# Optimization experiments

Measured on AMD Instinct MI355X. Metric: run time of the kernel, lower is better.

The kernel has to match this reference:

```python
import jax, jax.numpy as jnp
from jax import lax
import numpy as np

B, S, D = 4, 4096, 1024
ESCAPE_RADIUS = 2.0  # Mandelbrot-style escape bound used for per-row clamping
EPS = 1e-12


def setup_inputs() -> dict:
    key = jax.random.key(0)
    ks = jax.random.split(key, 6)
    x = jax.random.normal(ks[0], (B, S, D), dtype=jnp.float32)
    gamma = jnp.ones((D,), dtype=jnp.float32)
    beta = jnp.zeros((D,), dtype=jnp.float32)
    scale = 1.0 / np.sqrt(D)
    W_in = jax.random.normal(ks[1], (D, D), dtype=jnp.float32) * scale
    b_in = jnp.zeros((D,), dtype=jnp.float32)
    W_out = jax.random.normal(ks[2], (D, D), dtype=jnp.float32) * scale
    b_out = jnp.zeros((D,), dtype=jnp.float32)
    return {"x": x, "gamma": gamma, "beta": beta, "W_in": W_in,
            "b_in": b_in, "W_out": W_out, "b_out": b_out}


def _layernorm(x, gamma, beta):
    mu = jnp.mean(x, axis=-1, keepdims=True)
    var = jnp.mean((x - mu) ** 2, axis=-1, keepdims=True)
    return (x - mu) * lax.rsqrt(var + 1e-5) * gamma + beta


def _complex_square(z):
    # last dim = [real | imag] halves (torch chunk(2, dim=-1))
    re, im = jnp.split(z, 2, axis=-1)
    return jnp.concatenate([re * re - im * im, 2.0 * re * im], axis=-1)


def reference(x, gamma, beta, W_in, b_in, W_out, b_out):
    h = _layernorm(x, gamma, beta)
    c = jnp.einsum('bsd,de->bse', h, W_in) + b_in  # per-token complex offset

    def step(z, c_t):
        z_raw = _complex_square(z) + c_t
        # per-row L2 norm clamp to escape radius (keeps the chaotic map bounded)
        n = jnp.sqrt(jnp.sum(z_raw * z_raw, axis=-1, keepdims=True) + EPS)
        z_new = z_raw * (ESCAPE_RADIUS / jnp.maximum(n, ESCAPE_RADIUS))
        return z_new, z_new

    c_t_major = jnp.swapaxes(c, 0, 1)  # [S, B, D]
    z0 = jnp.zeros((x.shape[0], x.shape[-1]), dtype=x.dtype)
    _, ys = lax.scan(step, z0, c_t_major)  # ys: [S, B, D]
    y = jnp.swapaxes(ys, 0, 1)  # [B, S, D]
    out = jnp.einsum('bsd,de->bse', y, W_out) + b_out
    return x + out  # residual
```

## Files before the change

### kernel.cpp

```cpp
#include <hip/hip_runtime.h>

typedef __bf16 bf16_t;
typedef __bf16 bf16x8 __attribute__((ext_vector_type(8)));
typedef __bf16 bf16x4 __attribute__((ext_vector_type(4)));
typedef float  f32x4  __attribute__((ext_vector_type(4)));
typedef unsigned char u8;
typedef unsigned long long u64;

#define B_DIM 4
#define S_DIM 4096
#define D_DIM 1024
#define M_DIM (B_DIM * S_DIM)

#define CHUNK 32
#define WARM  16

__device__ __forceinline__ void g2l16(const void* g, void* l) {
  __builtin_amdgcn_global_load_lds(
      (const __attribute__((address_space(1))) void*)g,
      (__attribute__((address_space(3))) void*)l, 16, 0, 0);
}

__global__ __launch_bounds__(64) void ln_kernel(
    const float* __restrict__ x, const float* __restrict__ gamma,
    const float* __restrict__ beta, u8* __restrict__ h) {
  const int row  = blockIdx.x;
  const int lane = threadIdx.x;
  const float4* xr = (const float4*)(x + (size_t)row * D_DIM);
  float4 v[4];
  float s = 0.f, s2 = 0.f;
#pragma unroll
  for (int j = 0; j < 4; ++j) {
    v[j] = xr[j * 64 + lane];
    s += v[j].x + v[j].y + v[j].z + v[j].w;
    s2 = fmaf(v[j].x, v[j].x, s2);
    s2 = fmaf(v[j].y, v[j].y, s2);
    s2 = fmaf(v[j].z, v[j].z, s2);
    s2 = fmaf(v[j].w, v[j].w, s2);
  }
#pragma unroll
  for (int off = 32; off; off >>= 1) {
    s  += __shfl_xor(s, off);
    s2 += __shfl_xor(s2, off);
  }
  const float mu  = s * (1.f / (float)D_DIM);
  const float var = fmaf(-mu, mu, s2 * (1.f / (float)D_DIM));
  const float inv = rsqrtf(var + 1e-5f);
  int* hr = (int*)(h + (size_t)row * D_DIM);
#pragma unroll
  for (int j = 0; j < 4; ++j) {
    const float4 g4 = ((const float4*)gamma)[j * 64 + lane];
    const float4 b4 = ((const float4*)beta)[j * 64 + lane];
    const float o0 = fmaf((v[j].x - mu) * inv, g4.x, b4.x);
    const float o1 = fmaf((v[j].y - mu) * inv, g4.y, b4.y);
    const float o2 = fmaf((v[j].z - mu) * inv, g4.z, b4.z);
    const float o3 = fmaf((v[j].w - mu) * inv, g4.w, b4.w);
    int p = __builtin_amdgcn_cvt_pk_fp8_f32(o0, o1, 0, false);
    p = __builtin_amdgcn_cvt_pk_fp8_f32(o2, o3, p, true);
    hr[j * 64 + lane] = p;
  }
}

__global__ __launch_bounds__(256) void transpose_fp8_kernel(
    const float* __restrict__ W, u8* __restrict__ WT) {
  __shared__ float tile[32][33];
  const int tx = threadIdx.x & 31;
  const int ty = threadIdx.x >> 5;
  const int bn = blockIdx.x * 32;
  const int bk = blockIdx.y * 32;
#pragma unroll
  for (int i = 0; i < 32; i += 8)
    tile[ty + i][tx] = W[(size_t)(bk + ty + i) * D_DIM + bn + tx];
  __syncthreads();
#pragma unroll
  for (int i = 0; i < 32; i += 8) {
    const int p =
        __builtin_amdgcn_cvt_pk_fp8_f32(16.f * tile[tx][ty + i], 0.f, 0, false);
    WT[(size_t)(bn + ty + i) * D_DIM + bk + tx] = (u8)(p & 0xff);
  }
}

#define G1NT 16

template <int MODE>
__global__ __launch_bounds__(512, 4) void gemm_fp8_kernel(
    const u8* __restrict__ A, const u8* __restrict__ BT,
    const float* __restrict__ bias, const float* __restrict__ xres,
    void* __restrict__ Cout) {
  __shared__ __attribute__((aligned(16))) char lds[2][24576];
  const int tid  = threadIdx.x;
  const int lane = tid & 63;
  const int wave = tid >> 6;
  const int wr = wave >> 1;
  const int wc = wave & 1;
  const int bid = blockIdx.x;
  const int swz = (bid & 7) * 64 + (bid >> 3);
  const int m0 = (swz >> 3) * 256;
  const int n0 = (swz & 7) * 128;

  const int gs = ((tid & 3) ^ ((tid >> 3) & 3)) << 4;
  const u8* srcA = A  + (size_t)(m0 + (tid >> 2)) * D_DIM + gs;
  const u8* srcB = BT + (size_t)(n0 + (tid >> 2)) * D_DIM + gs;
  const int l16 = tid * 16;

  const int gg   = lane >> 4;
  const int arow = wr * 64 + (lane & 15);
  const int brow = wc * 64 + (lane & 15);
  const int aA0 = arow * 64 + ((((gg >> 1)) ^ ((arow >> 1) & 3)) << 4) + (gg & 1) * 8;
  const int bA0 = 16384 + brow * 64 +
                  ((((gg >> 1)) ^ ((brow >> 1) & 3)) << 4) + (gg & 1) * 8;

  f32x4 acc[4][4];
#pragma unroll
  for (int m = 0; m < 4; ++m)
#pragma unroll
    for (int n = 0; n < 4; ++n) acc[m][n] = (f32x4){0.f, 0.f, 0.f, 0.f};

#define STAGE(T)                                             \
  {                                                          \
    char* dst = lds[(T) & 1];                                \
    const size_t ko = (size_t)(T) * 64;                      \
    g2l16(srcA + ko, dst + l16);                             \
    g2l16(srcA + (size_t)128 * D_DIM + ko, dst + 8192 + l16);\
    g2l16(srcB + ko, dst + 16384 + l16);                     \
  }

  STAGE(0);
  for (int t = 0; t < G1NT; ++t) {
    __syncthreads();
    const char* buf = lds[t & 1];
    long a0[4], b0[4], a1[4], b1[4];
#pragma unroll
    for (int m = 0; m < 4; ++m)
      a0[m] = *(const long*)(buf + ((aA0 + m * 1024)));
#pragma unroll
    for (int n = 0; n < 4; ++n)
      b0[n] = *(const long*)(buf + ((bA0 + n * 1024)));
#pragma unroll
    for (int m = 0; m < 4; ++m)
      a1[m] = *(const long*)(buf + ((aA0 + m * 1024) ^ 32));
#pragma unroll
    for (int n = 0; n < 4; ++n)
      b1[n] = *(const long*)(buf + ((bA0 + n * 1024) ^ 32));
    if (t + 1 < G1NT) STAGE(t + 1);
#pragma unroll
    for (int m = 0; m < 4; ++m)
#pragma unroll
      for (int n = 0; n < 4; ++n)
        acc[m][n] = __builtin_amdgcn_mfma_f32_16x16x32_fp8_fp8(
            a0[m], b0[n], acc[m][n], 0, 0, 0);
#pragma unroll
    for (int m = 0; m < 4; ++m)
#pragma unroll
      for (int n = 0; n < 4; ++n)
        acc[m][n] = __builtin_amdgcn_mfma_f32_16x16x32_fp8_fp8(
            a1[m], b1[n], acc[m][n], 0, 0, 0);
  }
#undef STAGE

  const int rbase = m0 + wr * 64 + ((lane >> 4) << 2);
  const int cbase = n0 + wc * 64 + (lane & 15);
#pragma unroll
  for (int n = 0; n < 4; ++n) {
    const int col = cbase + n * 16;
    const float bn = bias[col];
#pragma unroll
    for (int m = 0; m < 4; ++m) {
      const int row = rbase + m * 16;
#pragma unroll
      for (int r = 0; r < 4; ++r) {
        const size_t idx = (size_t)(row + r) * D_DIM + col;
        if (MODE == 0) {
          const float cv = fmaf(acc[m][n][r], 0.0625f, bn);
          const int p = __builtin_amdgcn_cvt_pk_fp8_f32(cv, 0.f, 0, false);
          ((u8*)Cout)[idx] = (u8)(p & 0xff);
        } else {
          ((float*)Cout)[idx] =
              xres[idx] + fmaf(acc[m][n][r], 1.f / 256.f, bn);
        }
      }
    }
  }
}

__global__ __launch_bounds__(64) void scan_kernel(
    const u8* __restrict__ c, u8* __restrict__ y) {
  const int b     = blockIdx.y;
  const int chunk = blockIdx.x;
  const int t0    = chunk * CHUNK;
  const int start = (chunk == 0) ? 0 : t0 - WARM;
  const int tend  = t0 + CHUNK;
  const int lane  = threadIdx.x;

  float zre[8], zim[8];
#pragma unroll
  for (int j = 0; j < 8; ++j) { zre[j] = 0.f; zim[j] = 0.f; }

  const u8* crow = c + ((size_t)b * S_DIM + start) * D_DIM;
  u64 cr = *(const u64*)(crow + lane * 8);
  u64 ci = *(const u64*)(crow + 512 + lane * 8);

  for (int t = start; t < tend; ++t) {
    u64 crn = cr, cin = ci;
    if (t + 1 < tend) {
      const u8* nrow = c + ((size_t)b * S_DIM + (t + 1)) * D_DIM;
      crn = *(const u64*)(nrow + lane * 8);
      cin = *(const u64*)(nrow + 512 + lane * 8);
    }
    float cre[8], cim[8];
    {
      const unsigned rl = (unsigned)cr, rh = (unsigned)(cr >> 32);
      const unsigned il = (unsigned)ci, ih = (unsigned)(ci >> 32);
      cre[0] = __builtin_amdgcn_cvt_f32_fp8(rl, 0);
      cre[1] = __builtin_amdgcn_cvt_f32_fp8(rl, 1);
      cre[2] = __builtin_amdgcn_cvt_f32_fp8(rl, 2);
      cre[3] = __builtin_amdgcn_cvt_f32_fp8(rl, 3);
      cre[4] = __builtin_amdgcn_cvt_f32_fp8(rh, 0);
      cre[5] = __builtin_amdgcn_cvt_f32_fp8(rh, 1);
      cre[6] = __builtin_amdgcn_cvt_f32_fp8(rh, 2);
      cre[7] = __builtin_amdgcn_cvt_f32_fp8(rh, 3);
      cim[0] = __builtin_amdgcn_cvt_f32_fp8(il, 0);
      cim[1] = __builtin_amdgcn_cvt_f32_fp8(il, 1);
      cim[2] = __builtin_amdgcn_cvt_f32_fp8(il, 2);
      cim[3] = __builtin_amdgcn_cvt_f32_fp8(il, 3);
      cim[4] = __builtin_amdgcn_cvt_f32_fp8(ih, 0);
      cim[5] = __builtin_amdgcn_cvt_f32_fp8(ih, 1);
      cim[6] = __builtin_amdgcn_cvt_f32_fp8(ih, 2);
      cim[7] = __builtin_amdgcn_cvt_f32_fp8(ih, 3);
    }
    float nr[8], ni[8];
    float ss = 0.f;
#pragma unroll
    for (int j = 0; j < 8; ++j) {
      const float a  = zre[j], bb = zim[j];
      const float rr = fmaf(a, a, fmaf(-bb, bb, cre[j]));
      const float ii = fmaf(2.f * a, bb, cim[j]);
      nr[j] = rr; ni[j] = ii;
      ss = fmaf(rr, rr, ss);
      ss = fmaf(ii, ii, ss);
    }
#pragma unroll
    for (int off = 32; off; off >>= 1) ss += __shfl_xor(ss, off);
    const float nrm = sqrtf(ss + 1e-12f);
    const float sc  = 2.0f / fmaxf(nrm, 2.0f);
#pragma unroll
    for (int j = 0; j < 8; ++j) { zre[j] = nr[j] * sc; zim[j] = ni[j] * sc; }
    if (t >= t0) {
      u8* yrow = y + ((size_t)b * S_DIM + t) * D_DIM;
      int pr0 = __builtin_amdgcn_cvt_pk_fp8_f32(16.f * zre[0], 16.f * zre[1], 0, false);
      pr0 = __builtin_amdgcn_cvt_pk_fp8_f32(16.f * zre[2], 16.f * zre[3], pr0, true);
      int pr1 = __builtin_amdgcn_cvt_pk_fp8_f32(16.f * zre[4], 16.f * zre[5], 0, false);
      pr1 = __builtin_amdgcn_cvt_pk_fp8_f32(16.f * zre[6], 16.f * zre[7], pr1, true);
      int pi0 = __builtin_amdgcn_cvt_pk_fp8_f32(16.f * zim[0], 16.f * zim[1], 0, false);
      pi0 = __builtin_amdgcn_cvt_pk_fp8_f32(16.f * zim[2], 16.f * zim[3], pi0, true);
      int pi1 = __builtin_amdgcn_cvt_pk_fp8_f32(16.f * zim[4], 16.f * zim[5], 0, false);
      pi1 = __builtin_amdgcn_cvt_pk_fp8_f32(16.f * zim[6], 16.f * zim[7], pi1, true);
      *(u64*)(yrow + lane * 8)       = ((u64)(unsigned)pr1 << 32) | (unsigned)pr0;
      *(u64*)(yrow + 512 + lane * 8) = ((u64)(unsigned)pi1 << 32) | (unsigned)pi0;
    }
    cr = crn; ci = cin;
  }
}

extern "C" void kernel_launch(void* const* d_in, const int* in_sizes, int n_in,
                              void* d_out, int out_size, void* d_ws, size_t ws_size,
                              hipStream_t stream) {
  const float* x     = (const float*)d_in[0];
  const float* gamma = (const float*)d_in[1];
  const float* beta  = (const float*)d_in[2];
  const float* W_in  = (const float*)d_in[3];
  const float* b_in  = (const float*)d_in[4];
  const float* W_out = (const float*)d_in[5];
  const float* b_out = (const float*)d_in[6];
  float* out = (float*)d_out;

  char* ws = (char*)d_ws;
  u8* hy8  = (u8*)(ws);
  u8* c8   = (u8*)(ws + (16ull << 20));
  u8* wti8 = (u8*)(ws + (64ull << 20));
  u8* wto8 = (u8*)(ws + (65ull << 20));

  transpose_fp8_kernel<<<dim3(32, 32), 256, 0, stream>>>(W_in, wti8);
  transpose_fp8_kernel<<<dim3(32, 32), 256, 0, stream>>>(W_out, wto8);
  ln_kernel<<<M_DIM, 64, 0, stream>>>(x, gamma, beta, hy8);
  gemm_fp8_kernel<0><<<512, 512, 0, stream>>>(hy8, wti8, b_in, nullptr, c8);
  scan_kernel<<<dim3(S_DIM / CHUNK, B_DIM), 64, 0, stream>>>(c8, hy8);
  gemm_fp8_kernel<1><<<512, 512, 0, stream>>>(hy8, wto8, b_out, x, out);
}
```

Before: 132.2 us.

## Triple-buffer FP8 GEMM with permuted K layout and 128-bit LDS reads

The FP8 GEMM moves to a three-buffer global-to-LDS pipeline with explicit vmcnt waits, so loads run two stages ahead. The K dimension of both operands is permuted when written (in the layernorm, weight transpose and scan kernels), which lets each lane fetch both MFMA k-halves with one ds_read_b128. The block tile changes from 256x128 to 128x256 with a 2x4 wave grid. A hash-based s_sleep stagger at kernel start is added to spread memory traffic across blocks. The cost is more LDS per block, which may limit occupancy, plus the added startup delay.

```diff
diff --git a/kernel.cpp b/kernel.cpp
--- a/kernel.cpp
+++ b/kernel.cpp
@@ -1,9 +1,8 @@
 #include <hip/hip_runtime.h>
 
 typedef __bf16 bf16_t;
-typedef __bf16 bf16x8 __attribute__((ext_vector_type(8)));
-typedef __bf16 bf16x4 __attribute__((ext_vector_type(4)));
 typedef float  f32x4  __attribute__((ext_vector_type(4)));
+typedef long   longx2 __attribute__((ext_vector_type(2)));
 typedef unsigned char u8;
 typedef unsigned long long u64;
 
@@ -14,6 +13,10 @@
 
 #define CHUNK 32
 #define WARM  16
+
+__device__ __forceinline__ int pperm(int k) {
+  return (k & ~63) | (((k >> 3) & 3) << 4) | (((k >> 5) & 1) << 3) | (k & 7);
+}
 
 __device__ __forceinline__ void g2l16(const void* g, void* l) {
   __builtin_amdgcn_global_load_lds(
@@ -57,7 +60,7 @@
     const float o3 = fmaf((v[j].w - mu) * inv, g4.w, b4.w);
     int p = __builtin_amdgcn_cvt_pk_fp8_f32(o0, o1, 0, false);
     p = __builtin_amdgcn_cvt_pk_fp8_f32(o2, o3, p, true);
-    hr[j * 64 + lane] = p;
+    hr[pperm(j * 256 + lane * 4) >> 2] = p;
   }
 }
 
@@ -76,39 +79,46 @@
   for (int i = 0; i < 32; i += 8) {
     const int p =
         __builtin_amdgcn_cvt_pk_fp8_f32(16.f * tile[tx][ty + i], 0.f, 0, false);
-    WT[(size_t)(bn + ty + i) * D_DIM + bk + tx] = (u8)(p & 0xff);
-  }
-}
-
-#define G1NT 16
+    WT[(size_t)(bn + ty + i) * D_DIM + pperm(bk + tx)] = (u8)(p & 0xff);
+  }
+}
+
+#define NTK 16
+#define BUFSZ 24576
+
+#define VMCNT(n) asm volatile("s_waitcnt vmcnt(" #n ")" ::: "memory")
+#define DSRX(d, a, off) \
+  asm volatile("ds_read_b128 %0, %1 offset:" #off : "=v"(d) : "v"(a))
 
 template <int MODE>
 __global__ __launch_bounds__(512, 4) void gemm_fp8_kernel(
     const u8* __restrict__ A, const u8* __restrict__ BT,
     const float* __restrict__ bias, const float* __restrict__ xres,
     void* __restrict__ Cout) {
-  __shared__ __attribute__((aligned(16))) char lds[2][24576];
+  __shared__ __attribute__((aligned(16))) char lds[3][BUFSZ];
   const int tid  = threadIdx.x;
   const int lane = tid & 63;
   const int wave = tid >> 6;
-  const int wr = wave >> 1;
-  const int wc = wave & 1;
+  const int wr = wave >> 2;
+  const int wc = wave & 3;
   const int bid = blockIdx.x;
   const int swz = (bid & 7) * 64 + (bid >> 3);
-  const int m0 = (swz >> 3) * 256;
-  const int n0 = (swz & 7) * 128;
-
-  const int gs = ((tid & 3) ^ ((tid >> 3) & 3)) << 4;
-  const u8* srcA = A  + (size_t)(m0 + (tid >> 2)) * D_DIM + gs;
-  const u8* srcB = BT + (size_t)(n0 + (tid >> 2)) * D_DIM + gs;
+  const int m0 = (swz >> 2) * 128;
+  const int n0 = (swz & 3) * 256;
+
+  const int dly = (int)((bid * 2654435761u) >> 29);
+  for (int i = 0; i < dly; ++i) __builtin_amdgcn_s_sleep(1);
+
+  const int us = (((tid & 3) ^ ((tid >> 3) & 3)) << 4);
+  const u8* srcA = A  + (size_t)(m0 + (tid >> 2)) * D_DIM + us;
+  const u8* srcB = BT + (size_t)(n0 + (tid >> 2)) * D_DIM + us;
   const int l16 = tid * 16;
 
-  const int gg   = lane >> 4;
-  const int arow = wr * 64 + (lane & 15);
-  const int brow = wc * 64 + (lane & 15);
-  const int aA0 = arow * 64 + ((((gg >> 1)) ^ ((arow >> 1) & 3)) << 4) + (gg & 1) * 8;
-  const int bA0 = 16384 + brow * 64 +
-                  ((((gg >> 1)) ^ ((brow >> 1) & 3)) << 4) + (gg & 1) * 8;
+  const uint32_t lbase = (uint32_t)(uintptr_t)&lds[0][0];
+  const int sw = (((lane >> 4) ^ ((lane >> 1) & 3)) << 4);
+  const uint32_t aoff = lbase + (uint32_t)((wr * 64 + (lane & 15)) * 64 + sw);
+  const uint32_t boff = lbase + 8192u +
+                        (uint32_t)((wc * 64 + (lane & 15)) * 64 + sw);
 
   f32x4 acc[4][4];
 #pragma unroll
@@ -116,46 +126,56 @@
 #pragma unroll
     for (int n = 0; n < 4; ++n) acc[m][n] = (f32x4){0.f, 0.f, 0.f, 0.f};
 
-#define STAGE(T)                                             \
-  {                                                          \
-    char* dst = lds[(T) & 1];                                \
-    const size_t ko = (size_t)(T) * 64;                      \
-    g2l16(srcA + ko, dst + l16);                             \
-    g2l16(srcA + (size_t)128 * D_DIM + ko, dst + 8192 + l16);\
-    g2l16(srcB + ko, dst + 16384 + l16);                     \
-  }
-
-  STAGE(0);
-  for (int t = 0; t < G1NT; ++t) {
-    __syncthreads();
-    const char* buf = lds[t & 1];
-    long a0[4], b0[4], a1[4], b1[4];
-#pragma unroll
-    for (int m = 0; m < 4; ++m)
-      a0[m] = *(const long*)(buf + ((aA0 + m * 1024)));
-#pragma unroll
-    for (int n = 0; n < 4; ++n)
-      b0[n] = *(const long*)(buf + ((bA0 + n * 1024)));
-#pragma unroll
-    for (int m = 0; m < 4; ++m)
-      a1[m] = *(const long*)(buf + ((aA0 + m * 1024) ^ 32));
-#pragma unroll
-    for (int n = 0; n < 4; ++n)
-      b1[n] = *(const long*)(buf + ((bA0 + n * 1024) ^ 32));
-    if (t + 1 < G1NT) STAGE(t + 1);
-#pragma unroll
-    for (int m = 0; m < 4; ++m)
-#pragma unroll
-      for (int n = 0; n < 4; ++n)
-        acc[m][n] = __builtin_amdgcn_mfma_f32_16x16x32_fp8_fp8(
-            a0[m], b0[n], acc[m][n], 0, 0, 0);
-#pragma unroll
-    for (int m = 0; m < 4; ++m)
-#pragma unroll
-      for (int n = 0; n < 4; ++n)
-        acc[m][n] = __builtin_amdgcn_mfma_f32_16x16x32_fp8_fp8(
-            a1[m], b1[n], acc[m][n], 0, 0, 0);
-  }
+#define STAGE(T, BI)                                           \
+  {                                                            \
+    char* dst = (char*)lds + (BI) * BUFSZ;                     \
+    const size_t ko = (size_t)(T) * 64;                        \
+    g2l16(srcA + ko, dst + l16);                               \
+    g2l16(srcB + ko, dst + 8192 + l16);                        \
+    g2l16(srcB + (size_t)128 * D_DIM + ko, dst + 16384 + l16); \
+  }
+
+#define STEP_BODY(CUR, DO_STAGE, T)                                 \
+  {                                                                 \
+    __builtin_amdgcn_s_barrier();                                   \
+    const uint32_t bb = (uint32_t)(CUR) * BUFSZ;                    \
+    longx2 af[4], bf[4];                                            \
+    const uint32_t aA = aoff + bb;                                  \
+    DSRX(af[0], aA, 0);                                             \
+    DSRX(af[1], aA, 1024);                                          \
+    DSRX(af[2], aA, 2048);                                          \
+    DSRX(af[3], aA, 3072);                                          \
+    const uint32_t bA = boff + bb;                                  \
+    DSRX(bf[0], bA, 0);                                             \
+    DSRX(bf[1], bA, 1024);                                          \
+    DSRX(bf[2], bA, 2048);                                          \
+    DSRX(bf[3], bA, 3072);                                          \
+    if (DO_STAGE) { const int bi2 = (CUR) >= 1 ? (CUR) - 1 : (CUR) + 2; \
+                    STAGE((T) + 2, bi2); }                          \
+    asm volatile("s_waitcnt lgkmcnt(0)" ::: "memory");              \
+    __builtin_amdgcn_sched_barrier(0);                              \
+    _Pragma("unroll") for (int m = 0; m < 4; ++m)                   \
+        _Pragma("unroll") for (int n = 0; n < 4; ++n)               \
+            acc[m][n] = __builtin_amdgcn_mfma_f32_16x16x32_fp8_fp8( \
+                af[m][0], bf[n][0], acc[m][n], 0, 0, 0);            \
+    _Pragma("unroll") for (int m = 0; m < 4; ++m)                   \
+        _Pragma("unroll") for (int n = 0; n < 4; ++n)               \
+            acc[m][n] = __builtin_amdgcn_mfma_f32_16x16x32_fp8_fp8( \
+                af[m][1], bf[n][1], acc[m][n], 0, 0, 0);            \
+  }
+
+  STAGE(0, 0);
+  STAGE(1, 1);
+  int cur = 0;
+  for (int t = 0; t < NTK - 1; ++t) {
+    VMCNT(3);
+    STEP_BODY(cur, t + 2 < NTK, t);
+    cur = cur == 2 ? 0 : cur + 1;
+  }
+  VMCNT(0);
+  STEP_BODY(cur, false, NTK - 1);
+
+#undef STEP_BODY
 #undef STAGE
 
   const int rbase = m0 + wr * 64 + ((lane >> 4) << 2);
@@ -195,6 +215,10 @@
   float zre[8], zim[8];
 #pragma unroll
   for (int j = 0; j < 8; ++j) { zre[j] = 0.f; zim[j] = 0.f; }
+
+  const int dre = lane * 8;
+  const int pre = (dre & ~63) | (((dre >> 3) & 3) << 4) | (((dre >> 5) & 1) << 3);
+  const int pim = 512 + pre;
 
   const u8* crow = c + ((size_t)b * S_DIM + start) * D_DIM;
   u64 cr = *(const u64*)(crow + lane * 8);
@@ -255,8 +279,8 @@
       pi0 = __builtin_amdgcn_cvt_pk_fp8_f32(16.f * zim[2], 16.f * zim[3], pi0, true);
       int pi1 = __builtin_amdgcn_cvt_pk_fp8_f32(16.f * zim[4], 16.f * zim[5], 0, false);
       pi1 = __builtin_amdgcn_cvt_pk_fp8_f32(16.f * zim[6], 16.f * zim[7], pi1, true);
-      *(u64*)(yrow + lane * 8)       = ((u64)(unsigned)pr1 << 32) | (unsigned)pr0;
-      *(u64*)(yrow + 512 + lane * 8) = ((u64)(unsigned)pi1 << 32) | (unsigned)pi0;
+      *(u64*)(yrow + pre) = ((u64)(unsigned)pr1 << 32) | (unsigned)pr0;
+      *(u64*)(yrow + pim) = ((u64)(unsigned)pi1 << 32) | (unsigned)pi0;
     }
     cr = crn; ci = cin;
   }
```

After: 125.5 us. -5.1%, faster.

## Switch FP8 GEMMs to MI355 scaled MFMA 16x16x128 with retiled blocks

Applied to the files above, without the earlier changes.

Replaces the 16x16x32 fp8 MFMA GEMM with the gfx950 scaled f8f6f4 16x16x128 MFMA, passing a unit scale so the arithmetic stays plain FP8. The block tile changes from 256x128 with 512 threads to 128x128 with 256 threads, K steps widen to 128 bytes, and the LDS swizzle is redone for 128-byte rows. The aim is to raise matrix throughput per instruction and cut LDS reads. The smaller tiles mean more blocks and lower reuse per block.

```diff
diff --git a/kernel.cpp b/kernel.cpp
--- a/kernel.cpp
+++ b/kernel.cpp
@@ -1,9 +1,9 @@
 #include <hip/hip_runtime.h>
 
 typedef __bf16 bf16_t;
-typedef __bf16 bf16x8 __attribute__((ext_vector_type(8)));
-typedef __bf16 bf16x4 __attribute__((ext_vector_type(4)));
 typedef float  f32x4  __attribute__((ext_vector_type(4)));
+typedef int    i32x4  __attribute__((ext_vector_type(4)));
+typedef int    i32x8  __attribute__((ext_vector_type(8)));
 typedef unsigned char u8;
 typedef unsigned long long u64;
 
@@ -80,35 +80,44 @@
   }
 }
 
-#define G1NT 16
+#define NMX 8
+
+__device__ __forceinline__ i32x8 ldfrag(const char* region, int row, int g) {
+  const int x = row & 7;
+  const i32x4 lo =
+      *(const i32x4*)(region + row * 128 + ((((g << 1)) ^ x) << 4));
+  const i32x4 hi =
+      *(const i32x4*)(region + row * 128 + ((((g << 1) | 1) ^ x) << 4));
+  i32x8 r;
+  r[0] = lo[0]; r[1] = lo[1]; r[2] = lo[2]; r[3] = lo[3];
+  r[4] = hi[0]; r[5] = hi[1]; r[6] = hi[2]; r[7] = hi[3];
+  return r;
+}
 
 template <int MODE>
-__global__ __launch_bounds__(512, 4) void gemm_fp8_kernel(
+__global__ __launch_bounds__(256, 2) void gemm_mx_kernel(
     const u8* __restrict__ A, const u8* __restrict__ BT,
     const float* __restrict__ bias, const float* __restrict__ xres,
     void* __restrict__ Cout) {
-  __shared__ __attribute__((aligned(16))) char lds[2][24576];
+  __shared__ __attribute__((aligned(16))) char lds[2][32768];
   const int tid  = threadIdx.x;
   const int lane = tid & 63;
   const int wave = tid >> 6;
   const int wr = wave >> 1;
   const int wc = wave & 1;
   const int bid = blockIdx.x;
-  const int swz = (bid & 7) * 64 + (bid >> 3);
-  const int m0 = (swz >> 3) * 256;
+  const int swz = (bid & 7) * 128 + (bid >> 3);
+  const int m0 = (swz >> 3) * 128;
   const int n0 = (swz & 7) * 128;
 
-  const int gs = ((tid & 3) ^ ((tid >> 3) & 3)) << 4;
-  const u8* srcA = A  + (size_t)(m0 + (tid >> 2)) * D_DIM + gs;
-  const u8* srcB = BT + (size_t)(n0 + (tid >> 2)) * D_DIM + gs;
-  const int l16 = tid * 16;
-
-  const int gg   = lane >> 4;
-  const int arow = wr * 64 + (lane & 15);
-  const int brow = wc * 64 + (lane & 15);
-  const int aA0 = arow * 64 + ((((gg >> 1)) ^ ((arow >> 1) & 3)) << 4) + (gg & 1) * 8;
-  const int bA0 = 16384 + brow * 64 +
-                  ((((gg >> 1)) ^ ((brow >> 1) & 3)) << 4) + (gg & 1) * 8;
+  const int srow = tid >> 3;
+  const int us   = (((tid & 7) ^ (srow & 7)) << 4);
+  const u8* srcA = A  + (size_t)(m0 + srow) * D_DIM + us;
+  const u8* srcB = BT + (size_t)(n0 + srow) * D_DIM + us;
+  const int dst0 = tid * 16;
+
+  const int frow = lane & 15;
+  const int g    = lane >> 4;
 
   f32x4 acc[4][4];
 #pragma unroll
@@ -119,42 +128,36 @@
 #define STAGE(T)                                             \
   {                                                          \
     char* dst = lds[(T) & 1];                                \
-    const size_t ko = (size_t)(T) * 64;                      \
-    g2l16(srcA + ko, dst + l16);                             \
-    g2l16(srcA + (size_t)128 * D_DIM + ko, dst + 8192 + l16);\
-    g2l16(srcB + ko, dst + 16384 + l16);                     \
+    const size_t ko = (size_t)(T) * 128;                     \
+    g2l16(srcA + ko,                          dst + dst0);   \
+    g2l16(srcA + (size_t)32 * D_DIM + ko, dst + 4096 + dst0);  \
+    g2l16(srcA + (size_t)64 * D_DIM + ko, dst + 8192 + dst0);  \
+    g2l16(srcA + (size_t)96 * D_DIM + ko, dst + 12288 + dst0); \
+    g2l16(srcB + ko,                      dst + 16384 + dst0); \
+    g2l16(srcB + (size_t)32 * D_DIM + ko, dst + 20480 + dst0); \
+    g2l16(srcB + (size_t)64 * D_DIM + ko, dst + 24576 + dst0); \
+    g2l16(srcB + (size_t)96 * D_DIM + ko, dst + 28672 + dst0); \
   }
 
   STAGE(0);
-  for (int t = 0; t < G1NT; ++t) {
+  for (int t = 0; t < NMX; ++t) {
     __syncthreads();
     const char* buf = lds[t & 1];
-    long a0[4], b0[4], a1[4], b1[4];
+    i32x8 af[4], bf[4];
 #pragma unroll
     for (int m = 0; m < 4; ++m)
-      a0[m] = *(const long*)(buf + ((aA0 + m * 1024)));
+      af[m] = ldfrag(buf, wr * 64 + m * 16 + frow, g);
 #pragma unroll
     for (int n = 0; n < 4; ++n)
-      b0[n] = *(const long*)(buf + ((bA0 + n * 1024)));
+      bf[n] = ldfrag(buf + 16384, wc * 64 + n * 16 + frow, g);
+    if (t + 1 < NMX) STAGE(t + 1);
 #pragma unroll
     for (int m = 0; m < 4; ++m)
-      a1[m] = *(const long*)(buf + ((aA0 + m * 1024) ^ 32));
-#pragma unroll
-    for (int n = 0; n < 4; ++n)
-      b1[n] = *(const long*)(buf + ((bA0 + n * 1024) ^ 32));
-    if (t + 1 < G1NT) STAGE(t + 1);
-#pragma unroll
-    for (int m = 0; m < 4; ++m)
 #pragma unroll
       for (int n = 0; n < 4; ++n)
-        acc[m][n] = __builtin_amdgcn_mfma_f32_16x16x32_fp8_fp8(
-            a0[m], b0[n], acc[m][n], 0, 0, 0);
-#pragma unroll
-    for (int m = 0; m < 4; ++m)
-#pragma unroll
-      for (int n = 0; n < 4; ++n)
-        acc[m][n] = __builtin_amdgcn_mfma_f32_16x16x32_fp8_fp8(
-            a1[m], b1[n], acc[m][n], 0, 0, 0);
+        acc[m][n] = __builtin_amdgcn_mfma_scale_f32_16x16x128_f8f6f4(
+            af[m], bf[n], acc[m][n], 0, 0,
+            0, 0x7f7f7f7f, 0, 0x7f7f7f7f);
   }
 #undef STAGE
 
@@ -283,7 +286,7 @@
   transpose_fp8_kernel<<<dim3(32, 32), 256, 0, stream>>>(W_in, wti8);
   transpose_fp8_kernel<<<dim3(32, 32), 256, 0, stream>>>(W_out, wto8);
   ln_kernel<<<M_DIM, 64, 0, stream>>>(x, gamma, beta, hy8);
-  gemm_fp8_kernel<0><<<512, 512, 0, stream>>>(hy8, wti8, b_in, nullptr, c8);
+  gemm_mx_kernel<0><<<1024, 256, 0, stream>>>(hy8, wti8, b_in, nullptr, c8);
   scan_kernel<<<dim3(S_DIM / CHUNK, B_DIM), 64, 0, stream>>>(c8, hy8);
-  gemm_fp8_kernel<1><<<512, 512, 0, stream>>>(hy8, wto8, b_out, x, out);
-}
+  gemm_mx_kernel<1><<<1024, 256, 0, stream>>>(hy8, wto8, b_out, x, out);
+}
```

Measured after the change: 111.1 us. -16.0%, faster.
